# Kernel optimization log

Measured on AMD Instinct MI355X. Metric: run time of the kernel, lower is better.

The kernel has to match this reference:

```python
import jax, jax.numpy as jnp
import numpy as np

MUL = 32          # multiplicity of 0e and 1o in node/edge/out irreps
SQRT3 = np.sqrt(3.0).astype(np.float32)


def _split(x, mul):
    # x: [E, mul + mul*3] laid out as [mul x 0e | mul x 1o]
    s = x[:, :mul]
    v = x[:, mul:].reshape(x.shape[0], mul, 3)
    return s, v


def _mlp(x, W1, W2, W3):
    # e3nn-style FullyConnectedNet: no bias, 1/sqrt(fan_in) scaling, silu between layers
    h = jax.nn.silu(x @ (W1 / np.sqrt(np.float32(W1.shape[0]))))
    h = jax.nn.silu(h @ (W2 / np.sqrt(np.float32(W2.shape[0]))))
    return h @ (W3 / np.sqrt(np.float32(W3.shape[0])))


def _tp(s1, v1, s2, v2, W1, W2, W3, W4):
    # 'uvw' tensor product with irreps2 = 1x0e+1x1o (mul2 = 1).
    # CG paths: 0e*0e->0e, 0e*1o->1o, 1o*0e->1o, 1o*1o->0e (dot/sqrt(3)).
    alpha = 1.0 / np.sqrt(np.float32(s1.shape[1]))  # path norm 1/sqrt(mul1*mul2)
    out0a = jnp.einsum('uw,eu->ew', W1, s1 * s2[:, None]) * alpha
    out1a = jnp.einsum('uw,eu,em->ewm', W2, s1, v2) * alpha
    out1b = jnp.einsum('uw,eum->ewm', W3, v1 * s2[:, None, None]) * alpha
    dot = jnp.einsum('eum,em->eu', v1, v2) / SQRT3
    out0b = jnp.einsum('uw,eu->ew', W4, dot) * alpha
    # mid irreps (sorted+simplified): [2*MUL x 0e | 2*MUL x 1o]
    return jnp.concatenate([out0a, out0b], 1), jnp.concatenate([out1a, out1b], 1)


def _lin_scale(ms, mv, w):
    # LinearScaleWithWeights: per-edge generated weights, block per irrep
    E, U = ms.shape
    ws = w[:, :U * MUL].reshape(E, U, MUL)
    wv = w[:, U * MUL:].reshape(E, U, MUL)
    a = 1.0 / np.sqrt(np.float32(U))
    return (jnp.einsum('eu,euw->ew', ms, ws) * a,
            jnp.einsum('eum,euw->ewm', mv, wv) * a)


def _lin_out(s, v, Ls, Lv):
    # o3.Linear with internal shared weights, block-diagonal per irrep
    a = 1.0 / np.sqrt(np.float32(MUL))
    return s @ Ls * a, jnp.einsum('eum,uw->ewm', v, Lv) * a


def reference(node_feats_src, node_feats_dst, edge_feats, local_env_edge, edge_scalars,
              Wn_tp1, Wn_tp2, Wn_tp3, Wn_tp4, We_tp1, We_tp2, We_tp3, We_tp4,
              Wn_mlp1, Wn_mlp2, Wn_mlp3, We_mlp1, We_mlp2, We_mlp3,
              Lns, Lnv, Les, Lev):
    ss, sv = _split(node_feats_src, MUL)
    ds, dv = _split(node_feats_dst, MUL)
    # AttentionHeadsToVector over stacked (src, dst): concat heads along mul axis
    ns = jnp.concatenate([ss, ds], 1)     # [E, 64] (64x0e)
    nv = jnp.concatenate([sv, dv], 1)     # [E, 64, 3] (64x1o)
    es, ev = _split(edge_feats, MUL)
    ls = local_env_edge[:, 0]             # 1x0e
    lv = local_env_edge[:, 1:4]           # 1x1o
    # node branch
    wn = _mlp(edge_scalars, Wn_mlp1, Wn_mlp2, Wn_mlp3)   # [E, 4096]
    ms, mv = _tp(ns, nv, ls, lv, Wn_tp1, Wn_tp2, Wn_tp3, Wn_tp4)
    n_s, n_v = _lin_scale(ms, mv, wn)
    n_s, n_v = _lin_out(n_s, n_v, Lns, Lnv)
    # edge branch
    we = _mlp(edge_scalars, We_mlp1, We_mlp2, We_mlp3)   # [E, 4096]
    ms2, mv2 = _tp(es, ev, ls, lv, We_tp1, We_tp2, We_tp3, We_tp4)
    e_s, e_v = _lin_scale(ms2, mv2, we)
    e_s, e_v = _lin_out(e_s, e_v, Les, Lev)
    out_s = n_s + e_s
    out_v = n_v + e_v
    return jnp.concatenate([out_s, out_v.reshape(out_v.shape[0], -1)], 1)  # [E, 128]


def setup_inputs() -> dict:
    key = jax.random.key(0)
    ks = jax.random.split(key, 23)
    E = 30000
    rn = lambda k, shape: jax.random.normal(k, shape, dtype=jnp.float32)
    return {
        'node_feats_src': rn(ks[0], (E, 128)),
        'node_feats_dst': rn(ks[1], (E, 128)),
        'edge_feats': rn(ks[2], (E, 128)),
        'local_env_edge': rn(ks[3], (E, 4)),
        'edge_scalars': rn(ks[4], (E, 8)),
        'Wn_tp1': rn(ks[5], (64, 32)), 'Wn_tp2': rn(ks[6], (64, 32)),
        'Wn_tp3': rn(ks[7], (64, 32)), 'Wn_tp4': rn(ks[8], (64, 32)),
        'We_tp1': rn(ks[9], (32, 32)), 'We_tp2': rn(ks[10], (32, 32)),
        'We_tp3': rn(ks[11], (32, 32)), 'We_tp4': rn(ks[12], (32, 32)),
        'Wn_mlp1': rn(ks[13], (8, 64)), 'Wn_mlp2': rn(ks[14], (64, 64)),
        'Wn_mlp3': rn(ks[15], (64, 4096)),
        'We_mlp1': rn(ks[16], (8, 64)), 'We_mlp2': rn(ks[17], (64, 64)),
        'We_mlp3': rn(ks[18], (64, 4096)),
        'Lns': rn(ks[19], (32, 32)), 'Lnv': rn(ks[20], (32, 32)),
        'Les': rn(ks[21], (32, 32)), 'Lev': rn(ks[22], (32, 32)),
    }
```

## Files before the change

kernel.cpp:

```cpp
#include <hip/hip_runtime.h>

typedef __attribute__((ext_vector_type(8))) __bf16 bf16x8;
typedef __attribute__((ext_vector_type(4))) float f32x4;

#define MFMA16(A,B,C) __builtin_amdgcn_mfma_f32_16x16x32_bf16(A,B,C,0,0,0)

typedef const __attribute__((address_space(1))) void* gas_ptr;
typedef __attribute__((address_space(3))) void* las_ptr;

#define WS_W3N 0
#define WS_W3E 262144
#define WS_TN  524288
#define WS_TE  532480
#define WS_M1N 536576
#define WS_M2N 538624
#define WS_M1E 542720
#define WS_M2E 544768
#define WS_CNT 548864

__global__ void prep_kernel(
    const float* __restrict__ Wn1, const float* __restrict__ Wn2,
    const float* __restrict__ Wn3, const float* __restrict__ Wn4,
    const float* __restrict__ We1, const float* __restrict__ We2,
    const float* __restrict__ We3, const float* __restrict__ We4,
    const float* __restrict__ Mn1, const float* __restrict__ Mn2, const float* __restrict__ Mn3,
    const float* __restrict__ Me1, const float* __restrict__ Me2, const float* __restrict__ Me3,
    const float* __restrict__ Lns, const float* __restrict__ Lnv,
    const float* __restrict__ Les, const float* __restrict__ Lev,
    __bf16* __restrict__ ws)
{
  int idx = blockIdx.x * 256 + threadIdx.x;
  const float c1 = 0.0027621359f;
  const float an = 0.125f;
  const float ae = 0.17677669529663687f;
  const float r3 = 0.5773502691896258f;
  const float m1s = 0.35355339059327373f;
  const float m2s = 0.125f;
  if (idx < 524288) {
    int br = idx >> 18;
    int rem = idx & 262143;
    int j = rem >> 12;
    int kc = rem & 4095;
    int vh = kc >> 11;
    int r2 = kc & 2047;
    int u = r2 >> 5, wp = r2 & 31;
    const float* M3 = br ? Me3 : Mn3;
    const float* L  = vh ? (br ? Lev : Lnv) : (br ? Les : Lns);
    const float* mrow = M3 + (size_t)j * 4096 + vh * 2048 + u * 32;
    float s = 0.f;
    #pragma unroll
    for (int w = 0; w < 32; ++w) s += mrow[w] * L[w * 32 + wp];
    ws[(br ? WS_W3E : WS_W3N) + (size_t)kc * 64 + j] = (__bf16)(s * c1);
  } else if (idx < 524288 + 8192) {
    int t = idx - 524288;
    int i = t >> 11; int r = t & 2047; int w = r >> 6; int u = r & 63;
    const float* W = (i == 0) ? Wn1 : (i == 1) ? Wn2 : (i == 2) ? Wn3 : Wn4;
    float sc = an * ((i == 3) ? r3 : 1.f);
    ws[WS_TN + t] = (__bf16)(W[u * 32 + w] * sc);
  } else if (idx < 524288 + 12288) {
    int t = idx - 532480;
    int i = t >> 10; int r = t & 1023; int w = r >> 5; int u = r & 31;
    const float* W = (i == 0) ? We1 : (i == 1) ? We2 : (i == 2) ? We3 : We4;
    float sc = ae * ((i == 3) ? r3 : 1.f);
    ws[WS_TE + t] = (__bf16)(W[u * 32 + w] * sc);
  } else if (idx < 536576 + 2048) {
    int t = idx - 536576;
    int j = t >> 5, k = t & 31;
    ws[WS_M1N + t] = (__bf16)((k < 8) ? Mn1[k * 64 + j] * m1s : 0.f);
  } else if (idx < 538624 + 4096) {
    int t = idx - 538624;
    int j2 = t >> 6, j = t & 63;
    ws[WS_M2N + t] = (__bf16)(Mn2[j * 64 + j2] * m2s);
  } else if (idx < 542720 + 2048) {
    int t = idx - 542720;
    int j = t >> 5, k = t & 31;
    ws[WS_M1E + t] = (__bf16)((k < 8) ? Me1[k * 64 + j] * m1s : 0.f);
  } else if (idx < 544768 + 4096) {
    int t = idx - 544768;
    int j2 = t >> 6, j = t & 63;
    ws[WS_M2E + t] = (__bf16)(Me2[j * 64 + j2] * m2s);
  }
}

__device__ __forceinline__ float siluf(float x) { return x / (1.0f + __expf(-x)); }
__device__ __forceinline__ unsigned int pk2(float lo, float hi) {
  unsigned short a = __builtin_bit_cast(unsigned short, (__bf16)lo);
  unsigned short b = __builtin_bit_cast(unsigned short, (__bf16)hi);
  return (unsigned int)a | ((unsigned int)b << 16);
}
__device__ __forceinline__ float bflo(unsigned int v) { return __builtin_bit_cast(float, (unsigned int)(v << 16)); }
__device__ __forceinline__ float bfhi(unsigned int v) { return __builtin_bit_cast(float, (unsigned int)(v & 0xffff0000u)); }

__global__ __launch_bounds__(256, 2) void fused_kernel(
    const float* __restrict__ nsrc, const float* __restrict__ ndst,
    const float* __restrict__ efeat, const float* __restrict__ lenv,
    const float* __restrict__ escal,
    const __bf16* __restrict__ ws,
    float* __restrict__ out, int E)
{
  __shared__ __align__(16) char lds[81920];
  const int tid = threadIdx.x;
  const int wave = tid >> 6, l = tid & 63;
  const int lg = l >> 4, li = l & 15;
  const int ebase = blockIdx.x * 64;

  char* coeff = lds;
  char* h2n = lds + 32768;
  char* h2e = lds + 40960;

  const int uh = wave >> 1;
  const int ep = wave & 1;
  const int half = wave >> 1;
  const int rt_role = wave & 1;

  auto stage = [&](int buf, int branch, int b) {
    const char* gbase = (const char*)(ws + (branch ? WS_W3E : WS_W3N));
    char* dst = lds + 49152 + buf * 16384 + tid * 16;
    int row = tid >> 3, col = tid & 7;
    int roff = row * 128 + ((col ^ (row & 7)) << 4);
    #pragma unroll
    for (int r = 0; r < 4; ++r) {
      int u = b + (r >> 1) * 32, gv = r & 1;
      const char* src = gbase + gv * 262144 + u * 4096 + roff;
      __builtin_amdgcn_global_load_lds((gas_ptr)src, (las_ptr)(dst + r * 4096), 16, 0, 0);
    }
  };

  {
    const int br = wave >> 1;
    const __bf16* M1 = ws + (br ? WS_M1E : WS_M1N);
    const __bf16* M2 = ws + (br ? WS_M2E : WS_M2N);
    char* h2buf = br ? h2e : h2n;
    char* h1s = lds + wave * 8192;
    #pragma unroll 1
    for (int c2 = 0; c2 < 2; ++c2) {
      int ct = (wave & 1) * 2 + c2;
      int el = ct * 16 + li;
      int hl = c2 * 16 + li;
      int ee = min(ebase + el, E - 1);
      bf16x8 bx;
      #pragma unroll
      for (int i = 0; i < 8; ++i) bx[i] = (__bf16)0.f;
      if (lg == 0) {
        const float* xp = escal + (size_t)ee * 8;
        float4 t0 = *(const float4*)(xp);
        float4 t1 = *(const float4*)(xp + 4);
        bx[0]=(__bf16)t0.x; bx[1]=(__bf16)t0.y; bx[2]=(__bf16)t0.z; bx[3]=(__bf16)t0.w;
        bx[4]=(__bf16)t1.x; bx[5]=(__bf16)t1.y; bx[6]=(__bf16)t1.z; bx[7]=(__bf16)t1.w;
      }
      f32x4 hc[4];
      #pragma unroll
      for (int rt = 0; rt < 4; ++rt) {
        bf16x8 a = *(const bf16x8*)(M1 + (rt * 16 + li) * 32 + lg * 8);
        f32x4 c = {0.f, 0.f, 0.f, 0.f};
        hc[rt] = MFMA16(a, bx, c);
      }
      #pragma unroll
      for (int rt = 0; rt < 4; ++rt) {
        int j0 = rt * 16 + lg * 4;
        int g = j0 >> 3;
        int addr = hl * 128 + (((g ^ (hl & 7)) << 4)) + (j0 & 7) * 2;
        uint2 wv; wv.x = pk2(siluf(hc[rt][0]), siluf(hc[rt][1]));
        wv.y = pk2(siluf(hc[rt][2]), siluf(hc[rt][3]));
        *(uint2*)(h1s + addr) = wv;
      }
      f32x4 h2c[4];
      #pragma unroll
      for (int rt = 0; rt < 4; ++rt) { f32x4 z = {0.f,0.f,0.f,0.f}; h2c[rt] = z; }
      #pragma unroll
      for (int kj = 0; kj < 2; ++kj) {
        bf16x8 b = *(const bf16x8*)(h1s + hl * 128 + (((kj * 4 + lg) ^ (hl & 7)) << 4));
        #pragma unroll
        for (int rt = 0; rt < 4; ++rt) {
          bf16x8 a = *(const bf16x8*)(M2 + (rt * 16 + li) * 64 + kj * 32 + lg * 8);
          h2c[rt] = MFMA16(a, b, h2c[rt]);
        }
      }
      #pragma unroll
      for (int rt = 0; rt < 4; ++rt) {
        int j0 = rt * 16 + lg * 4;
        int g = j0 >> 3;
        int addr = el * 128 + (((g ^ (el & 7)) << 4)) + (j0 & 7) * 2;
        uint2 wv; wv.x = pk2(siluf(h2c[rt][0]), siluf(h2c[rt][1]));
        wv.y = pk2(siluf(h2c[rt][2]), siluf(h2c[rt][3]));
        *(uint2*)(h2buf + addr) = wv;
      }
    }
  }
  __syncthreads();

  auto q_phase = [&](const float* f0, const float* f1, int nk, const __bf16* T, int ustride) {
    #pragma unroll 1
    for (int ct = 0; ct < 4; ++ct) {
      int el = ct * 16 + li;
      int ee = min(ebase + el, E - 1);
      const float4 le = *(const float4*)(lenv + (size_t)ee * 4);
      const size_t erow = (size_t)ee * 128;
      if (half == 0) {
        f32x4 q1c = {0.f,0.f,0.f,0.f}, q2c = {0.f,0.f,0.f,0.f};
        for (int kj = 0; kj < nk; ++kj) {
          const float* fp = (kj ? f1 : f0) + erow + lg * 8;
          float4 t0 = *(const float4*)(fp);
          float4 t1 = *(const float4*)(fp + 4);
          bf16x8 b;
          b[0]=(__bf16)t0.x; b[1]=(__bf16)t0.y; b[2]=(__bf16)t0.z; b[3]=(__bf16)t0.w;
          b[4]=(__bf16)t1.x; b[5]=(__bf16)t1.y; b[6]=(__bf16)t1.z; b[7]=(__bf16)t1.w;
          bf16x8 a1 = *(const bf16x8*)(T + (rt_role * 16 + li) * ustride + kj * 32 + lg * 8);
          bf16x8 a2 = *(const bf16x8*)(T + 32 * ustride + (rt_role * 16 + li) * ustride + kj * 32 + lg * 8);
          q1c = MFMA16(a1, b, q1c);
          q2c = MFMA16(a2, b, q2c);
        }
        #pragma unroll
        for (int r = 0; r < 4; ++r) {
          uint2 cw;
          cw.x = pk2(q1c[r] * le.x, q2c[r] * le.y);
          cw.y = pk2(q2c[r] * le.z, q2c[r] * le.w);
          *(uint2*)(coeff + (rt_role * 16 + lg * 4 + r) * 512 + el * 8) = cw;
        }
      } else {
        f32x4 q30 = {0.f,0.f,0.f,0.f}, q31 = {0.f,0.f,0.f,0.f}, q32 = {0.f,0.f,0.f,0.f}, q4c = {0.f,0.f,0.f,0.f};
        for (int kj = 0; kj < nk; ++kj) {
          const float* fp = (kj ? f1 : f0) + erow + 32 + lg * 24;
          float v[24];
          #pragma unroll
          for (int q = 0; q < 6; ++q) {
            float4 t = *(const float4*)(fp + q * 4);
            v[q*4] = t.x; v[q*4+1] = t.y; v[q*4+2] = t.z; v[q*4+3] = t.w;
          }
          bf16x8 b0, b1, b2, bd;
          #pragma unroll
          for (int i = 0; i < 8; ++i) {
            b0[i] = (__bf16)v[3*i]; b1[i] = (__bf16)v[3*i+1]; b2[i] = (__bf16)v[3*i+2];
            bd[i] = (__bf16)(v[3*i] * le.y + v[3*i+1] * le.z + v[3*i+2] * le.w);
          }
          bf16x8 a3 = *(const bf16x8*)(T + 2 * 32 * ustride + (rt_role * 16 + li) * ustride + kj * 32 + lg * 8);
          bf16x8 a4 = *(const bf16x8*)(T + 3 * 32 * ustride + (rt_role * 16 + li) * ustride + kj * 32 + lg * 8);
          q30 = MFMA16(a3, b0, q30); q31 = MFMA16(a3, b1, q31); q32 = MFMA16(a3, b2, q32);
          q4c = MFMA16(a4, bd, q4c);
        }
        #pragma unroll
        for (int r = 0; r < 4; ++r) {
          uint2 cw;
          cw.x = pk2(q4c[r], q30[r] * le.x);
          cw.y = pk2(q31[r] * le.x, q32[r] * le.x);
          *(uint2*)(coeff + (32 + rt_role * 16 + lg * 4 + r) * 512 + el * 8) = cw;
        }
      }
    }
  };

  f32x4 aS[2][2], aV[2][2][3];
  #pragma unroll
  for (int t2 = 0; t2 < 2; ++t2)
    #pragma unroll
    for (int rt = 0; rt < 2; ++rt) {
      f32x4 z = {0.f,0.f,0.f,0.f};
      aS[t2][rt] = z;
      aV[t2][rt][0] = z; aV[t2][rt][1] = z; aV[t2][rt][2] = z;
    }

  bf16x8 bb[2][2];
  auto load_bb = [&](char* h2buf) {
    #pragma unroll
    for (int t2 = 0; t2 < 2; ++t2)
      #pragma unroll
      for (int kj = 0; kj < 2; ++kj) {
        int el = (ep * 2 + t2) * 16 + li;
        bb[t2][kj] = *(const bf16x8*)(h2buf + el * 128 + (((kj * 4 + lg) ^ (el & 7)) << 4));
      }
  };

  auto main_block = [&](int buf, int b) {
    const char* afb = lds + 49152 + buf * 16384 + uh * 8192;
    int u_rel = uh * 32 + b;
    uint2 cf0 = *(const uint2*)(coeff + u_rel * 512 + ((ep * 2) * 16 + li) * 8);
    uint2 cf1 = *(const uint2*)(coeff + u_rel * 512 + ((ep * 2 + 1) * 16 + li) * 8);
    bf16x8 afS[2][2], afV[2][2];
    #pragma unroll
    for (int rt = 0; rt < 2; ++rt)
      #pragma unroll
      for (int kj = 0; kj < 2; ++kj) {
        int off = (rt * 16 + li) * 128 + (((kj * 4 + lg) ^ (li & 7)) << 4);
        afS[rt][kj] = *(const bf16x8*)(afb + off);
        afV[rt][kj] = *(const bf16x8*)(afb + 4096 + off);
      }
    #pragma unroll
    for (int t2 = 0; t2 < 2; ++t2) {
      uint2 cf = t2 ? cf1 : cf0;
      float ms = bflo(cf.x), m0 = bfhi(cf.x), m1 = bflo(cf.y), m2 = bfhi(cf.y);
      #pragma unroll
      for (int rt = 0; rt < 2; ++rt) {
        f32x4 c = {0.f,0.f,0.f,0.f};
        c = MFMA16(afS[rt][0], bb[t2][0], c);
        c = MFMA16(afS[rt][1], bb[t2][1], c);
        aS[t2][rt] += ms * c;
        f32x4 d = {0.f,0.f,0.f,0.f};
        d = MFMA16(afV[rt][0], bb[t2][0], d);
        d = MFMA16(afV[rt][1], bb[t2][1], d);
        aV[t2][rt][0] += m0 * d;
        aV[t2][rt][1] += m1 * d;
        aV[t2][rt][2] += m2 * d;
      }
    }
  };

  stage(0, 0, 0);
  q_phase(nsrc, ndst, 2, ws + WS_TN, 64);
  __syncthreads();

  load_bb(h2n);
  #pragma unroll 1
  for (int b = 0; b < 32; ++b) {
    if (b < 31) stage((b + 1) & 1, 0, b + 1);
    else        stage(0, 1, 0);
    main_block(b & 1, b);
    __syncthreads();
  }

  q_phase(efeat, efeat, 1, ws + WS_TE, 32);
  __syncthreads();

  load_bb(h2e);
  #pragma unroll 1
  for (int b = 0; b < 32; ++b) {
    if (b < 31) stage((b + 1) & 1, 1, b + 1);
    main_block(b & 1, b);
    __syncthreads();
  }

  char* R1 = lds;
  auto rmw = [&](bool add) {
    #pragma unroll
    for (int t2 = 0; t2 < 2; ++t2) {
      int e = (ep * 2 + t2) * 16 + li;
      char* epp = R1 + e * 512;
      #pragma unroll
      for (int rt = 0; rt < 2; ++rt) {
        f32x4 s = aS[t2][rt];
        char* p = epp + (((rt * 4 + lg) ^ (e & 7)) << 4);
        if (add) s += *(const f32x4*)p;
        *(f32x4*)p = s;
        #pragma unroll
        for (int m = 0; m < 3; ++m) {
          f32x4 x = aV[t2][rt][m];
          char* q = epp + (((8 + m * 8 + rt * 4 + lg) ^ (e & 7)) << 4);
          if (add) x += *(const f32x4*)q;
          *(f32x4*)q = x;
        }
      }
    }
  };
  if (uh == 0) rmw(false);
  __syncthreads();
  if (uh == 1) rmw(true);
  __syncthreads();

  #pragma unroll
  for (int it = 0; it < 8; ++it) {
    int chunk = it * 256 + tid;
    int e = chunk >> 5, c4 = chunk & 31;
    f32x4 v;
    #pragma unroll
    for (int q = 0; q < 4; ++q) {
      int f = c4 * 4 + q;
      int g, wd;
      if (f < 32) { g = f >> 2; wd = f & 3; }
      else { int t = f - 32; int w = t / 3; int m = t - w * 3; g = 8 + m * 8 + (w >> 2); wd = w & 3; }
      v[q] = *(const float*)(R1 + e * 512 + ((g ^ (e & 7)) << 4) + wd * 4);
    }
    int ge = ebase + e;
    if (ge < E) *(f32x4*)(out + (size_t)ge * 128 + c4 * 4) = v;
  }
}

extern "C" void kernel_launch(void* const* d_in, const int* in_sizes, int n_in,
                              void* d_out, int out_size, void* d_ws, size_t ws_size,
                              hipStream_t stream) {
  const float* nsrc  = (const float*)d_in[0];
  const float* ndst  = (const float*)d_in[1];
  const float* efeat = (const float*)d_in[2];
  const float* lenv  = (const float*)d_in[3];
  const float* escal = (const float*)d_in[4];
  const float* Wn1 = (const float*)d_in[5];
  const float* Wn2 = (const float*)d_in[6];
  const float* Wn3 = (const float*)d_in[7];
  const float* Wn4 = (const float*)d_in[8];
  const float* We1 = (const float*)d_in[9];
  const float* We2 = (const float*)d_in[10];
  const float* We3 = (const float*)d_in[11];
  const float* We4 = (const float*)d_in[12];
  const float* Mn1 = (const float*)d_in[13];
  const float* Mn2 = (const float*)d_in[14];
  const float* Mn3 = (const float*)d_in[15];
  const float* Me1 = (const float*)d_in[16];
  const float* Me2 = (const float*)d_in[17];
  const float* Me3 = (const float*)d_in[18];
  const float* Lns = (const float*)d_in[19];
  const float* Lnv = (const float*)d_in[20];
  const float* Les = (const float*)d_in[21];
  const float* Lev = (const float*)d_in[22];
  (void)n_in; (void)ws_size;

  int E = in_sizes[0] / 128;
  __bf16* ws = (__bf16*)d_ws;
  float* outp = (float*)d_out;
  (void)out_size;

  int nprep = (WS_CNT + 255) / 256;
  hipLaunchKernelGGL(prep_kernel, dim3(nprep), dim3(256), 0, stream,
                     Wn1, Wn2, Wn3, Wn4, We1, We2, We3, We4,
                     Mn1, Mn2, Mn3, Me1, Me2, Me3,
                     Lns, Lnv, Les, Lev, ws);

  int nwg = (E + 63) / 64;
  hipLaunchKernelGGL(fused_kernel, dim3(nwg), dim3(256), 0, stream,
                     nsrc, ndst, efeat, lenv, escal, ws, outp, E);
}
```

Measured before the change: 76.59 us.

## Deepen weight prefetch pipeline and shrink LDS to raise occupancy

Both h2 activation tiles are loaded into registers up front, so their LDS region can be reused for the double-buffered weight staging. This cuts the shared memory allocation from 80 KB to 64 KB. The prefetch now runs two blocks ahead, with split barriers and a partial vmcnt wait in place of a full syncthreads, so global-to-LDS loads overlap more of the MFMA work. The cost is extra registers for the two h2 copies and more hand-managed synchronisation, which is fragile if the count of outstanding loads is wrong.

```diff
diff --git a/kernel.cpp b/kernel.cpp
--- a/kernel.cpp
+++ b/kernel.cpp
@@ -7,6 +7,9 @@
 
 typedef const __attribute__((address_space(1))) void* gas_ptr;
 typedef __attribute__((address_space(3))) void* las_ptr;
+
+#define BARRIER() do { asm volatile("" ::: "memory"); __builtin_amdgcn_s_barrier(); asm volatile("" ::: "memory"); } while (0)
+#define WAIT_VM4() asm volatile("s_waitcnt vmcnt(4)" ::: "memory")
 
 #define WS_W3N 0
 #define WS_W3E 262144
@@ -98,15 +101,16 @@
     const __bf16* __restrict__ ws,
     float* __restrict__ out, int E)
 {
-  __shared__ __align__(16) char lds[81920];
+  __shared__ __align__(16) char lds[65536];
   const int tid = threadIdx.x;
   const int wave = tid >> 6, l = tid & 63;
   const int lg = l >> 4, li = l & 15;
   const int ebase = blockIdx.x * 64;
 
   char* coeff = lds;
-  char* h2n = lds + 32768;
-  char* h2e = lds + 40960;
+  char* afbase = lds + 32768;
+  char* h2n = afbase;
+  char* h2e = afbase + 8192;
 
   const int uh = wave >> 1;
   const int ep = wave & 1;
@@ -115,7 +119,7 @@
 
   auto stage = [&](int buf, int branch, int b) {
     const char* gbase = (const char*)(ws + (branch ? WS_W3E : WS_W3N));
-    char* dst = lds + 49152 + buf * 16384 + tid * 16;
+    char* dst = afbase + buf * 16384 + tid * 16;
     int row = tid >> 3, col = tid & 7;
     int roff = row * 128 + ((col ^ (row & 7)) << 4);
     #pragma unroll
@@ -187,6 +191,18 @@
       }
     }
   }
+  __syncthreads();
+
+  bf16x8 bbN[2][2], bbE[2][2];
+  #pragma unroll
+  for (int t2 = 0; t2 < 2; ++t2)
+    #pragma unroll
+    for (int kj = 0; kj < 2; ++kj) {
+      int el = (ep * 2 + t2) * 16 + li;
+      int off = el * 128 + (((kj * 4 + lg) ^ (el & 7)) << 4);
+      bbN[t2][kj] = *(const bf16x8*)(h2n + off);
+      bbE[t2][kj] = *(const bf16x8*)(h2e + off);
+    }
   __syncthreads();
 
   auto q_phase = [&](const float* f0, const float* f1, int nk, const __bf16* T, int ustride) {
@@ -259,19 +275,8 @@
       aV[t2][rt][0] = z; aV[t2][rt][1] = z; aV[t2][rt][2] = z;
     }
 
-  bf16x8 bb[2][2];
-  auto load_bb = [&](char* h2buf) {
-    #pragma unroll
-    for (int t2 = 0; t2 < 2; ++t2)
-      #pragma unroll
-      for (int kj = 0; kj < 2; ++kj) {
-        int el = (ep * 2 + t2) * 16 + li;
-        bb[t2][kj] = *(const bf16x8*)(h2buf + el * 128 + (((kj * 4 + lg) ^ (el & 7)) << 4));
-      }
-  };
-
-  auto main_block = [&](int buf, int b) {
-    const char* afb = lds + 49152 + buf * 16384 + uh * 8192;
+  auto main_block = [&](int buf, int b, const bf16x8 (&bb)[2][2]) {
+    const char* afb = afbase + buf * 16384 + uh * 8192;
     int u_rel = uh * 32 + b;
     uint2 cf0 = *(const uint2*)(coeff + u_rel * 512 + ((ep * 2) * 16 + li) * 8);
     uint2 cf1 = *(const uint2*)(coeff + u_rel * 512 + ((ep * 2 + 1) * 16 + li) * 8);
@@ -305,27 +310,30 @@
   };
 
   stage(0, 0, 0);
+  stage(1, 0, 1);
   q_phase(nsrc, ndst, 2, ws + WS_TN, 64);
   __syncthreads();
 
-  load_bb(h2n);
   #pragma unroll 1
   for (int b = 0; b < 32; ++b) {
-    if (b < 31) stage((b + 1) & 1, 0, b + 1);
-    else        stage(0, 1, 0);
-    main_block(b & 1, b);
-    __syncthreads();
+    main_block(b & 1, b, bbN);
+    BARRIER();
+    if (b < 30)      stage(b & 1, 0, b + 2);
+    else             stage(b & 1, 1, b - 30);
+    WAIT_VM4();
+    BARRIER();
   }
 
   q_phase(efeat, efeat, 1, ws + WS_TE, 32);
   __syncthreads();
 
-  load_bb(h2e);
   #pragma unroll 1
   for (int b = 0; b < 32; ++b) {
-    if (b < 31) stage((b + 1) & 1, 1, b + 1);
-    main_block(b & 1, b);
-    __syncthreads();
+    main_block(b & 1, b, bbE);
+    BARRIER();
+    if (b < 30) stage(b & 1, 1, b + 2);
+    WAIT_VM4();
+    BARRIER();
   }
 
   char* R1 = lds;
```

Result: faster. 72.88 us (-4.8%).
